# Optimization experiments

Measured on AMD Instinct MI355X. Metric: run time of the kernel, lower is better.

## Reference

```python
import jax, jax.numpy as jnp
import numpy as np

E = 8          # n_routed_experts
TOP_K = 2      # num_experts_per_tok
H = 1024       # hidden_size
I = 512        # moe_intermediate_size
SI = 512       # shared expert intermediate (I * n_shared_experts)
B, S = 4, 4096


def setup_inputs() -> dict:
    key = jax.random.key(0)
    ks = jax.random.split(key, 8)
    sc_h = 1.0 / np.sqrt(H)
    sc_i = 1.0 / np.sqrt(I)
    return {
        "hidden_states": jax.random.normal(ks[0], (B, S, H), jnp.float32),
        "gate_w": jax.random.normal(ks[1], (E, H), jnp.float32) * sc_h,  # router logits weight [E,H]
        "Wg": jax.random.normal(ks[2], (E, H, I), jnp.float32) * sc_h,   # per-expert gate_proj
        "Wu": jax.random.normal(ks[3], (E, H, I), jnp.float32) * sc_h,   # per-expert up_proj
        "Wd": jax.random.normal(ks[4], (E, I, H), jnp.float32) * sc_i,   # per-expert down_proj
        "sWg": jax.random.normal(ks[5], (H, SI), jnp.float32) * sc_h,    # shared expert gate_proj
        "sWu": jax.random.normal(ks[6], (H, SI), jnp.float32) * sc_h,
        "sWd": jax.random.normal(ks[7], (SI, H), jnp.float32) * sc_i,
    }


def reference(hidden_states, gate_w, Wg, Wu, Wd, sWg, sWu, sWd):
    b, s, h = hidden_states.shape
    x = hidden_states.reshape(-1, h)                      # [T,H]

    # ---- MoEGate: softmax scoring + greedy top-k + weight normalization ----
    logits = x.astype(jnp.float32) @ gate_w.T             # [T,E]
    scores = jax.nn.softmax(logits, axis=-1)
    topk_w, topk_idx = jax.lax.top_k(scores, TOP_K)       # [T,K]
    topk_w = topk_w / (topk_w.sum(-1, keepdims=True) + 1e-20)  # norm_topk_prob

    # combine weights as a dense [T,E] map (scatter of topk weights)
    cw = (jax.nn.one_hot(topk_idx, E, dtype=topk_w.dtype) * topk_w[..., None]).sum(1)  # [T,E]

    # ---- routed experts: down(gelu(gate(x)) * up(x)), combined by gate weight ----
    g = jnp.einsum("th,ehi->tei", x, Wg)
    u = jnp.einsum("th,ehi->tei", x, Wu)
    inter = jax.nn.gelu(g, approximate=False) * u         # [T,E,I]
    y = jnp.einsum("tei,te,eih->th", inter, cw.astype(x.dtype), Wd)

    # ---- shared expert on the identity path ----
    sh = (jax.nn.gelu(x @ sWg, approximate=False) * (x @ sWu)) @ sWd

    return (y + sh).reshape(b, s, h)
```

## Files before the change

### kernel.cpp

```cpp
#include <hip/hip_runtime.h>
#include <hip/hip_bf16.h>
#include <math.h>


#define T_TOTAL 16384
#define HDIM 1024
#define IDIM 512
#define NE 9
#define CNT_STRIDE 16
#define SH_BASE 32768

typedef __bf16 bf16x8 __attribute__((ext_vector_type(8)));
typedef float f32x4 __attribute__((ext_vector_type(4)));

typedef __attribute__((address_space(1))) void gvoid_t;
typedef __attribute__((address_space(3))) void lvoid_t;

__device__ __forceinline__ void load_lds16(const void* g, void* l) {
  __builtin_amdgcn_global_load_lds((const gvoid_t*)g, (lvoid_t*)l, 16, 0, 0);
}

__device__ __forceinline__ f32x4 mfma_bf16(bf16x8 a, bf16x8 b, f32x4 c) {
  return __builtin_amdgcn_mfma_f32_16x16x32_bf16(a, b, c, 0, 0, 0);
}

__global__ __launch_bounds__(256) void k_gate(const float* __restrict__ x,
                                              const float* __restrict__ gw,
                                              __bf16* __restrict__ xb,
                                              int* __restrict__ tok,
                                              float* __restrict__ wtl,
                                              int* __restrict__ cnt,
                                              int* __restrict__ inv) {
  __shared__ int s_eid[64][2];
  __shared__ float s_wt[64][2];
  __shared__ int s_rank[64][2];
  __shared__ int lcnt[8];
  __shared__ int lbase[8];
  const int wv = threadIdx.x >> 6, lane = threadIdx.x & 63;
  if (threadIdx.x < 8) lcnt[threadIdx.x] = 0;
  __syncthreads();

  for (int i = 0; i < 16; i++) {
    const int tl = wv * 16 + i;
    const int t = blockIdx.x * 64 + tl;
    const float* xr = x + (size_t)t * HDIM + lane * 16;
    float4 xv[4];
#pragma unroll
    for (int j = 0; j < 4; j++) xv[j] = ((const float4*)xr)[j];

    bf16x8 v0, v1;
#pragma unroll
    for (int j = 0; j < 8; j++) v0[j] = (__bf16)((const float*)xv)[j];
#pragma unroll
    for (int j = 0; j < 8; j++) v1[j] = (__bf16)((const float*)xv)[j + 8];
    bf16x8* xbo = (bf16x8*)(xb + (size_t)t * HDIM + lane * 16);
    xbo[0] = v0;
    xbo[1] = v1;

    float acc[8];
#pragma unroll
    for (int e = 0; e < 8; e++) {
      const float4* gp = (const float4*)(gw + e * HDIM + lane * 16);
      float s = 0.f;
#pragma unroll
      for (int j = 0; j < 4; j++) {
        float4 g = gp[j];
        s += xv[j].x * g.x + xv[j].y * g.y + xv[j].z * g.z + xv[j].w * g.w;
      }
      acc[e] = s;
    }
#pragma unroll
    for (int d = 32; d >= 1; d >>= 1) {
#pragma unroll
      for (int e = 0; e < 8; e++) acc[e] += __shfl_xor(acc[e], d, 64);
    }
    if (lane == 0) {
      float mx = acc[0];
#pragma unroll
      for (int e = 1; e < 8; e++) mx = fmaxf(mx, acc[e]);
      float p[8], Z = 0.f;
#pragma unroll
      for (int e = 0; e < 8; e++) {
        p[e] = expf(acc[e] - mx);
        Z += p[e];
      }
#pragma unroll
      for (int e = 0; e < 8; e++) p[e] /= Z;
      int i1 = 0;
#pragma unroll
      for (int e = 1; e < 8; e++)
        if (p[e] > p[i1]) i1 = e;
      int i2 = (i1 == 0) ? 1 : 0;
#pragma unroll
      for (int e = 0; e < 8; e++)
        if (e != i1 && p[e] > p[i2]) i2 = e;
      const float s12 = p[i1] + p[i2] + 1e-20f;
      s_eid[tl][0] = i1;
      s_eid[tl][1] = i2;
      s_wt[tl][0] = p[i1] / s12;
      s_wt[tl][1] = p[i2] / s12;
    }
  }
  __syncthreads();

  if (threadIdx.x < 64) {
    s_rank[threadIdx.x][0] = atomicAdd(&lcnt[s_eid[threadIdx.x][0]], 1);
    s_rank[threadIdx.x][1] = atomicAdd(&lcnt[s_eid[threadIdx.x][1]], 1);
  }
  __syncthreads();
  if (threadIdx.x < 8)
    lbase[threadIdx.x] =
        atomicAdd(&cnt[threadIdx.x * CNT_STRIDE], lcnt[threadIdx.x]);
  __syncthreads();
  if (threadIdx.x < 64) {
    const int t = blockIdx.x * 64 + threadIdx.x;
#pragma unroll
    for (int j = 0; j < 2; j++) {
      const int e = s_eid[threadIdx.x][j];
      const int slot = lbase[e] + s_rank[threadIdx.x][j];
      tok[e * T_TOTAL + slot] = t;
      wtl[e * T_TOTAL + slot] = s_wt[threadIdx.x][j];
      inv[t * 2 + j] = e * T_TOTAL + slot;
    }
  }
}

__global__ __launch_bounds__(256) void k_wprep(
    const float* __restrict__ Wg, const float* __restrict__ Wu,
    const float* __restrict__ Wd, const float* __restrict__ sWg,
    const float* __restrict__ sWu, const float* __restrict__ sWd,
    __bf16* __restrict__ Wfu, __bf16* __restrict__ WdT,
    const int* __restrict__ cnt, int* __restrict__ base) {
  if (blockIdx.z == 26 && blockIdx.x == 0 && blockIdx.y == 0 &&
      threadIdx.x == 0) {
    int s = 0;
#pragma unroll
    for (int e = 0; e < 8; e++) {
      base[e] = s;
      s += cnt[e * CNT_STRIDE];
    }
  }

  __shared__ float tile[64][65];
  const int z = blockIdx.z;
  const int t = threadIdx.x;

  if (z < 18) {
    if (blockIdx.x >= IDIM / 64) return;
    const int b = (z < 9) ? z : z - 9;
    const int u16off = (z < 9) ? 0 : 16;
    const float* w8 = (z < 9) ? Wg : Wu;
    const float* w1 = (z < 9) ? sWg : sWu;
    const float* src = (b < 8) ? (w8 + (size_t)b * HDIM * IDIM) : w1;
    const int c0 = blockIdx.x * 64, r0 = blockIdx.y * 64;

#pragma unroll
    for (int j = 0; j < 4; j++) {
      const int rr = (t >> 4) + j * 16;
      const int cc = (t & 15) * 4;
      const float4 v =
          *(const float4*)(src + (size_t)(r0 + rr) * IDIM + c0 + cc);
      tile[rr][cc] = v.x;
      tile[rr][cc + 1] = v.y;
      tile[rr][cc + 2] = v.z;
      tile[rr][cc + 3] = v.w;
    }
    __syncthreads();

#pragma unroll
    for (int j = 0; j < 2; j++) {
      const int cidx = (t >> 3) + j * 32;
      const int rseg = (t & 7) * 8;
      const int ic = c0 + cidx;
      const int f = 2 * (ic & ~15) + (ic & 15) + u16off;
      bf16x8 v;
#pragma unroll
      for (int k = 0; k < 8; k++) v[k] = (__bf16)tile[rseg + k][cidx];
      *(bf16x8*)(Wfu + (size_t)b * 1024 * HDIM + (size_t)f * HDIM + r0 + rseg) =
          v;
    }
  } else {
    if (blockIdx.y >= IDIM / 64) return;
    const int b = z - 18;
    const float* src = (b < 8) ? (Wd + (size_t)b * IDIM * HDIM) : sWd;
    const int c0 = blockIdx.x * 64, r0 = blockIdx.y * 64;

#pragma unroll
    for (int j = 0; j < 4; j++) {
      const int rr = (t >> 4) + j * 16;
      const int cc = (t & 15) * 4;
      const float4 v =
          *(const float4*)(src + (size_t)(r0 + rr) * HDIM + c0 + cc);
      tile[rr][cc] = v.x;
      tile[rr][cc + 1] = v.y;
      tile[rr][cc + 2] = v.z;
      tile[rr][cc + 3] = v.w;
    }
    __syncthreads();

#pragma unroll
    for (int j = 0; j < 2; j++) {
      const int cidx = (t >> 3) + j * 32;
      const int rseg = (t & 7) * 8;
      bf16x8 v;
#pragma unroll
      for (int k = 0; k < 8; k++) v[k] = (__bf16)tile[rseg + k][cidx];
      *(bf16x8*)(WdT + (size_t)b * HDIM * IDIM + (size_t)(c0 + cidx) * IDIM +
                 r0 + rseg) = v;
    }
  }
}

__global__ __launch_bounds__(256, 2) void k_gu(
    const __bf16* __restrict__ xb, const __bf16* __restrict__ Wfu,
    const int* __restrict__ tok, const float* __restrict__ wtl,
    const int* __restrict__ cnt, const int* __restrict__ base,
    __bf16* __restrict__ inter, int zbase) {
  const int e = blockIdx.z + zbase;
  const bool se = (e == 8);
  const int cnt_e = se ? T_TOTAL : cnt[e * CNT_STRIDE];
  const int m0 = blockIdx.x * 128;
  if (m0 >= cnt_e) return;
  const int rowb = se ? SH_BASE : base[e];

  __shared__ __bf16 sA[128][64];
  __shared__ __bf16 sB[128][64];
  const int tid = threadIdx.x, w = tid >> 6, lane = tid & 63;
  const int n0 = blockIdx.y * 128;
  const int quad = lane >> 4, l16 = lane & 15;
  const int wm = (w & 1) * 64, wn = (w >> 1) * 64;

  const int sr = tid >> 3;
  const int scs = ((tid & 7) ^ (sr & 7)) * 8;
  const __bf16* ap[4];
  const __bf16* bp[4];
#pragma unroll
  for (int sh = 0; sh < 4; sh++) {
    int s = m0 + sh * 32 + sr;
    if (s > cnt_e - 1) s = cnt_e - 1;
    const int t = se ? s : tok[e * T_TOTAL + s];
    ap[sh] = xb + (size_t)t * HDIM + scs;
    bp[sh] = Wfu + ((size_t)e * 1024 + n0 + sh * 32 + sr) * HDIM + scs;
  }
  char* const la = (char*)sA + w * 1024;
  char* const lb = (char*)sB + w * 1024;

  f32x4 acc[4][4];
#pragma unroll
  for (int im = 0; im < 4; im++)
#pragma unroll
    for (int in = 0; in < 4; in++) acc[im][in] = {0.f, 0.f, 0.f, 0.f};

  for (int k = 0; k < HDIM; k += 64) {
    __syncthreads();
#pragma unroll
    for (int sh = 0; sh < 4; sh++) {
      load_lds16(ap[sh], la + sh * 4096);
      load_lds16(bp[sh], lb + sh * 4096);
      ap[sh] += 64;
      bp[sh] += 64;
    }
    __syncthreads();
#pragma unroll
    for (int kh = 0; kh < 2; kh++) {
      bf16x8 af[4], bfr[4];
#pragma unroll
      for (int i = 0; i < 4; i++) {
        const int ra = wm + i * 16 + l16;
        af[i] = *(const bf16x8*)((const char*)sA + ra * 128 +
                                 ((kh * 4 + quad) ^ (ra & 7)) * 16);
        const int rb = wn + i * 16 + l16;
        bfr[i] = *(const bf16x8*)((const char*)sB + rb * 128 +
                                  ((kh * 4 + quad) ^ (rb & 7)) * 16);
      }
#pragma unroll
      for (int im = 0; im < 4; im++)
#pragma unroll
        for (int in = 0; in < 4; in++)
          acc[im][in] = mfma_bf16(af[im], bfr[in], acc[im][in]);
    }
  }

#pragma unroll
  for (int im = 0; im < 4; im++) {
#pragma unroll
    for (int r = 0; r < 4; r++) {
      const int slot = m0 + wm + im * 16 + quad * 4 + r;
      if (slot < cnt_e) {
        const float wt = se ? 1.0f : wtl[e * T_TOTAL + slot];
        __bf16* op =
            inter + ((size_t)(rowb + slot)) * IDIM + ((n0 + wn) >> 1) + l16;
#pragma unroll
        for (int p = 0; p < 2; p++) {
          const float g = acc[im][2 * p][r];
          const float u = acc[im][2 * p + 1][r];
          const float v =
              wt * u * 0.5f * g * (1.0f + erff(g * 0.70710678118654752f));
          op[p * 16] = (__bf16)v;
        }
      }
    }
  }
}

__global__ __launch_bounds__(256, 2) void k_down_rs(
    const __bf16* __restrict__ inter, const __bf16* __restrict__ WdT,
    const int* __restrict__ cnt, const int* __restrict__ base,
    f32x4* __restrict__ yb4) {
  const int e = blockIdx.z;
  const int cnt_e = cnt[e * CNT_STRIDE];
  const int m0 = blockIdx.x * 128;
  if (m0 >= cnt_e) return;
  const int rowb = base[e];

  __shared__ __bf16 sA[128][64];
  __shared__ __bf16 sB[128][64];
  const int tid = threadIdx.x, w = tid >> 6, lane = tid & 63;
  const int n0 = blockIdx.y * 128;
  const int quad = lane >> 4, l16 = lane & 15;
  const int wm = (w & 1) * 64, wn = (w >> 1) * 64;
  const int nseg = (n0 + wn) >> 6;

  const int sr = tid >> 3;
  const int scs = ((tid & 7) ^ (sr & 7)) * 8;
  const __bf16* ap[4];
  const __bf16* bp[4];
#pragma unroll
  for (int sh = 0; sh < 4; sh++) {
    int s = m0 + sh * 32 + sr;
    if (s > cnt_e - 1) s = cnt_e - 1;
    ap[sh] = inter + (size_t)(rowb + s) * IDIM + scs;
    bp[sh] = WdT + ((size_t)e * HDIM + n0 + sh * 32 + sr) * IDIM + scs;
  }
  char* const la = (char*)sA + w * 1024;
  char* const lb = (char*)sB + w * 1024;

  f32x4 acc[4][4];
#pragma unroll
  for (int im = 0; im < 4; im++)
#pragma unroll
    for (int in = 0; in < 4; in++) acc[im][in] = {0.f, 0.f, 0.f, 0.f};

  for (int k = 0; k < IDIM; k += 64) {
    __syncthreads();
#pragma unroll
    for (int sh = 0; sh < 4; sh++) {
      load_lds16(ap[sh], la + sh * 4096);
      load_lds16(bp[sh], lb + sh * 4096);
      ap[sh] += 64;
      bp[sh] += 64;
    }
    __syncthreads();
#pragma unroll
    for (int kh = 0; kh < 2; kh++) {
      bf16x8 af[4], bfr[4];
#pragma unroll
      for (int i = 0; i < 4; i++) {
        const int ra = wm + i * 16 + l16;
        af[i] = *(const bf16x8*)((const char*)sA + ra * 128 +
                                 ((kh * 4 + quad) ^ (ra & 7)) * 16);
        const int rb = wn + i * 16 + l16;
        bfr[i] = *(const bf16x8*)((const char*)sB + rb * 128 +
                                  ((kh * 4 + quad) ^ (rb & 7)) * 16);
      }
#pragma unroll
      for (int im = 0; im < 4; im++)
#pragma unroll
        for (int in = 0; in < 4; in++)
          acc[im][in] = mfma_bf16(af[im], bfr[in], acc[im][in]);
    }
  }

#pragma unroll
  for (int im = 0; im < 4; im++) {
#pragma unroll
    for (int r = 0; r < 4; r++) {
      const int slot = m0 + wm + im * 16 + quad * 4 + r;
      if (slot < cnt_e) {
        const size_t row = (size_t)(rowb + slot);
        f32x4 v = {acc[im][0][r], acc[im][1][r], acc[im][2][r], acc[im][3][r]};
        yb4[(row * 16 + nseg) * 16 + l16] = v;
      }
    }
  }
}

__global__ __launch_bounds__(256, 2) void k_down_sc(
    const __bf16* __restrict__ iA, const __bf16* __restrict__ wB,
    const f32x4* __restrict__ yb4, const int* __restrict__ inv,
    const int* __restrict__ base, float* __restrict__ out) {
  __shared__ __bf16 sA[128][64];
  __shared__ __bf16 sB[128][64];
  const int tid = threadIdx.x, w = tid >> 6, lane = tid & 63;
  const int m0 = blockIdx.x * 128, n0 = blockIdx.y * 128;
  const int quad = lane >> 4, l16 = lane & 15;
  const int wm = (w & 1) * 64, wn = (w >> 1) * 64;
  const int nseg = (n0 + wn) >> 6;

  const int sr = tid >> 3;
  const int scs = ((tid & 7) ^ (sr & 7)) * 8;
  const __bf16* ap[4];
  const __bf16* bp[4];
#pragma unroll
  for (int sh = 0; sh < 4; sh++) {
    ap[sh] = iA + (size_t)(m0 + sh * 32 + sr) * IDIM + scs;
    bp[sh] = wB + (size_t)(n0 + sh * 32 + sr) * IDIM + scs;
  }
  char* const la = (char*)sA + w * 1024;
  char* const lb = (char*)sB + w * 1024;

  f32x4 acc[4][4];
#pragma unroll
  for (int im = 0; im < 4; im++)
#pragma unroll
    for (int in = 0; in < 4; in++) acc[im][in] = {0.f, 0.f, 0.f, 0.f};

  for (int k = 0; k < IDIM; k += 64) {
    __syncthreads();
#pragma unroll
    for (int sh = 0; sh < 4; sh++) {
      load_lds16(ap[sh], la + sh * 4096);
      load_lds16(bp[sh], lb + sh * 4096);
      ap[sh] += 64;
      bp[sh] += 64;
    }
    __syncthreads();
#pragma unroll
    for (int kh = 0; kh < 2; kh++) {
      bf16x8 af[4], bfr[4];
#pragma unroll
      for (int i = 0; i < 4; i++) {
        const int ra = wm + i * 16 + l16;
        af[i] = *(const bf16x8*)((const char*)sA + ra * 128 +
                                 ((kh * 4 + quad) ^ (ra & 7)) * 16);
        const int rb = wn + i * 16 + l16;
        bfr[i] = *(const bf16x8*)((const char*)sB + rb * 128 +
                                  ((kh * 4 + quad) ^ (rb & 7)) * 16);
      }
#pragma unroll
      for (int im = 0; im < 4; im++)
#pragma unroll
        for (int in = 0; in < 4; in++)
          acc[im][in] = mfma_bf16(af[im], bfr[in], acc[im][in]);
    }
  }

#pragma unroll
  for (int im = 0; im < 4; im++) {
#pragma unroll
    for (int r = 0; r < 4; r++) {
      const int t = m0 + wm + im * 16 + quad * 4 + r;
      const int v1 = inv[2 * t], v2 = inv[2 * t + 1];
      const size_t r1 = base[v1 >> 14] + (v1 & (T_TOTAL - 1));
      const size_t r2 = base[v2 >> 14] + (v2 & (T_TOTAL - 1));
      const f32x4 y1 = yb4[(r1 * 16 + nseg) * 16 + l16];
      const f32x4 y2 = yb4[(r2 * 16 + nseg) * 16 + l16];
      float* op = out + (size_t)t * HDIM + n0 + wn + l16;
#pragma unroll
      for (int in = 0; in < 4; in++)
        op[in * 16] = acc[im][in][r] + y1[in] + y2[in];
    }
  }
}

__global__ __launch_bounds__(256, 2) void k_down_s(const __bf16* __restrict__ iA,
                                                   const __bf16* __restrict__ wB,
                                                   float* __restrict__ out) {
  __shared__ __bf16 sA[128][64];
  __shared__ __bf16 sB[128][64];
  const int tid = threadIdx.x, w = tid >> 6, lane = tid & 63;
  const int m0 = blockIdx.x * 128, n0 = blockIdx.y * 128;
  const int quad = lane >> 4, l16 = lane & 15;
  const int wm = (w & 1) * 64, wn = (w >> 1) * 64;

  const int sr = tid >> 3;
  const int scs = ((tid & 7) ^ (sr & 7)) * 8;
  const __bf16* ap[4];
  const __bf16* bp[4];
#pragma unroll
  for (int sh = 0; sh < 4; sh++) {
    ap[sh] = iA + (size_t)(m0 + sh * 32 + sr) * IDIM + scs;
    bp[sh] = wB + (size_t)(n0 + sh * 32 + sr) * IDIM + scs;
  }
  char* const la = (char*)sA + w * 1024;
  char* const lb = (char*)sB + w * 1024;

  f32x4 acc[4][4];
#pragma unroll
  for (int im = 0; im < 4; im++)
#pragma unroll
    for (int in = 0; in < 4; in++) acc[im][in] = {0.f, 0.f, 0.f, 0.f};

  for (int k = 0; k < IDIM; k += 64) {
    __syncthreads();
#pragma unroll
    for (int sh = 0; sh < 4; sh++) {
      load_lds16(ap[sh], la + sh * 4096);
      load_lds16(bp[sh], lb + sh * 4096);
      ap[sh] += 64;
      bp[sh] += 64;
    }
    __syncthreads();
#pragma unroll
    for (int kh = 0; kh < 2; kh++) {
      bf16x8 af[4], bfr[4];
#pragma unroll
      for (int i = 0; i < 4; i++) {
        const int ra = wm + i * 16 + l16;
        af[i] = *(const bf16x8*)((const char*)sA + ra * 128 +
                                 ((kh * 4 + quad) ^ (ra & 7)) * 16);
        const int rb = wn + i * 16 + l16;
        bfr[i] = *(const bf16x8*)((const char*)sB + rb * 128 +
                                  ((kh * 4 + quad) ^ (rb & 7)) * 16);
      }
#pragma unroll
      for (int im = 0; im < 4; im++)
#pragma unroll
        for (int in = 0; in < 4; in++)
          acc[im][in] = mfma_bf16(af[im], bfr[in], acc[im][in]);
    }
  }

#pragma unroll
  for (int im = 0; im < 4; im++) {
#pragma unroll
    for (int r = 0; r < 4; r++) {
      const int t = m0 + wm + im * 16 + quad * 4 + r;
#pragma unroll
      for (int in = 0; in < 4; in++)
        out[(size_t)t * HDIM + n0 + wn + in * 16 + l16] = acc[im][in][r];
    }
  }
}

__global__ __launch_bounds__(256, 2) void k_down_r(
    const __bf16* __restrict__ inter, const __bf16* __restrict__ WdT,
    const int* __restrict__ tok, const int* __restrict__ cnt,
    const int* __restrict__ base, float* __restrict__ out) {
  const int e = blockIdx.z;
  const int cnt_e = cnt[e * CNT_STRIDE];
  const int m0 = blockIdx.x * 128;
  if (m0 >= cnt_e) return;
  const int rowb = base[e];

  __shared__ __bf16 sA[128][64];
  __shared__ __bf16 sB[128][64];
  const int tid = threadIdx.x, w = tid >> 6, lane = tid & 63;
  const int n0 = blockIdx.y * 128;
  const int quad = lane >> 4, l16 = lane & 15;
  const int wm = (w & 1) * 64, wn = (w >> 1) * 64;

  const int sr = tid >> 3;
  const int scs = ((tid & 7) ^ (sr & 7)) * 8;
  const __bf16* ap[4];
  const __bf16* bp[4];
#pragma unroll
  for (int sh = 0; sh < 4; sh++) {
    int s = m0 + sh * 32 + sr;
    if (s > cnt_e - 1) s = cnt_e - 1;
    ap[sh] = inter + (size_t)(rowb + s) * IDIM + scs;
    bp[sh] = WdT + ((size_t)e * HDIM + n0 + sh * 32 + sr) * IDIM + scs;
  }
  char* const la = (char*)sA + w * 1024;
  char* const lb = (char*)sB + w * 1024;

  f32x4 acc[4][4];
#pragma unroll
  for (int im = 0; im < 4; im++)
#pragma unroll
    for (int in = 0; in < 4; in++) acc[im][in] = {0.f, 0.f, 0.f, 0.f};

  for (int k = 0; k < IDIM; k += 64) {
    __syncthreads();
#pragma unroll
    for (int sh = 0; sh < 4; sh++) {
      load_lds16(ap[sh], la + sh * 4096);
      load_lds16(bp[sh], lb + sh * 4096);
      ap[sh] += 64;
      bp[sh] += 64;
    }
    __syncthreads();
#pragma unroll
    for (int kh = 0; kh < 2; kh++) {
      bf16x8 af[4], bfr[4];
#pragma unroll
      for (int i = 0; i < 4; i++) {
        const int ra = wm + i * 16 + l16;
        af[i] = *(const bf16x8*)((const char*)sA + ra * 128 +
                                 ((kh * 4 + quad) ^ (ra & 7)) * 16);
        const int rb = wn + i * 16 + l16;
        bfr[i] = *(const bf16x8*)((const char*)sB + rb * 128 +
                                  ((kh * 4 + quad) ^ (rb & 7)) * 16);
      }
#pragma unroll
      for (int im = 0; im < 4; im++)
#pragma unroll
        for (int in = 0; in < 4; in++)
          acc[im][in] = mfma_bf16(af[im], bfr[in], acc[im][in]);
    }
  }

#pragma unroll
  for (int im = 0; im < 4; im++) {
#pragma unroll
    for (int r = 0; r < 4; r++) {
      const int slot = m0 + wm + im * 16 + quad * 4 + r;
      if (slot < cnt_e) {
        const int t = tok[e * T_TOTAL + slot];
#pragma unroll
        for (int in = 0; in < 4; in++)
          atomicAdd(&out[(size_t)t * HDIM + n0 + wn + in * 16 + l16],
                    acc[im][in][r]);
      }
    }
  }
}

extern "C" void kernel_launch(void* const* d_in, const int* in_sizes, int n_in,
                              void* d_out, int out_size, void* d_ws,
                              size_t ws_size, hipStream_t stream) {
  const float* x = (const float*)d_in[0];
  const float* gw = (const float*)d_in[1];
  const float* Wg = (const float*)d_in[2];
  const float* Wu = (const float*)d_in[3];
  const float* Wd = (const float*)d_in[4];
  const float* sWg = (const float*)d_in[5];
  const float* sWu = (const float*)d_in[6];
  const float* sWd = (const float*)d_in[7];
  float* out = (float*)d_out;

  char* ws = (char*)d_ws;
  size_t off = 0;
  auto alloc = [&](size_t n) {
    char* p = ws + off;
    off += (n + 255) & ~(size_t)255;
    return p;
  };
  __bf16* WdT = (__bf16*)alloc((size_t)NE * HDIM * IDIM * 2);
  int* tok = (int*)alloc((size_t)8 * T_TOTAL * 4);
  float* wtl = (float*)alloc((size_t)8 * T_TOTAL * 4);
  int* cnt = (int*)alloc(8 * CNT_STRIDE * 4);
  int* inv = (int*)alloc((size_t)T_TOTAL * 2 * 4);
  int* base = (int*)alloc(16 * 4);
  __bf16* inter = (__bf16*)alloc((size_t)(3 * T_TOTAL) * IDIM * 2);
  const size_t off_persist = off;
  __bf16* xb = (__bf16*)alloc((size_t)T_TOTAL * HDIM * 2);
  __bf16* Wfu = (__bf16*)alloc((size_t)NE * 1024 * HDIM * 2);

  const size_t yb_bytes = (size_t)2 * T_TOTAL * HDIM * 4;
  const bool store_path = (off_persist + yb_bytes) <= ws_size;
  f32x4* yb4 = (f32x4*)(ws + off_persist);

  hipMemsetAsync(cnt, 0, 8 * CNT_STRIDE * 4, stream);

  k_gate<<<dim3(T_TOTAL / 64), dim3(256), 0, stream>>>(x, gw, xb, tok, wtl,
                                                       cnt, inv);
  k_wprep<<<dim3(16, 16, 27), dim3(256), 0, stream>>>(Wg, Wu, Wd, sWg, sWu,
                                                      sWd, Wfu, WdT, cnt, base);

  k_gu<<<dim3(T_TOTAL / 128, 1024 / 128, 4), dim3(256), 0, stream>>>(
      xb, Wfu, tok, wtl, cnt, base, inter, 0);
  k_gu<<<dim3(T_TOTAL / 128, 1024 / 128, 4), dim3(256), 0, stream>>>(
      xb, Wfu, tok, wtl, cnt, base, inter, 4);
  k_gu<<<dim3(T_TOTAL / 128, 1024 / 128, 1), dim3(256), 0, stream>>>(
      xb, Wfu, tok, wtl, cnt, base, inter, 8);

  if (store_path) {
    k_down_rs<<<dim3(T_TOTAL / 128, HDIM / 128, 8), dim3(256), 0, stream>>>(
        inter, WdT, cnt, base, yb4);
    k_down_sc<<<dim3(T_TOTAL / 128, HDIM / 128), dim3(256), 0, stream>>>(
        inter + (size_t)SH_BASE * IDIM, WdT + (size_t)8 * HDIM * IDIM, yb4, inv,
        base, out);
  } else {
    k_down_s<<<dim3(T_TOTAL / 128, HDIM / 128), dim3(256), 0, stream>>>(
        inter + (size_t)SH_BASE * IDIM, WdT + (size_t)8 * HDIM * IDIM, out);
    k_down_r<<<dim3(T_TOTAL / 128, HDIM / 128, 8), dim3(256), 0, stream>>>(
        inter, WdT, tok, cnt, base, out);
  }
}
```

Baseline: 450.0 us.

## Scatter routed down-proj outputs by token slot and merge gate-up launches

Routed expert down-projection results are now written into a token-ordered buffer indexed by (token, k-slot), with the k-slot packed into the high bits of the tok array. The combine kernel no longer needs the inverse map or the base offsets, and it reads both expert contributions contiguously instead of gathering them. The three gate/up launches are merged into one grid over all nine experts. The trade-off is scattered writes in the routed kernel in exchange for coalesced reads in the combine step, plus one fewer index array and fewer launches.

```diff
diff --git a/kernel.cpp b/kernel.cpp
--- a/kernel.cpp
+++ b/kernel.cpp
@@ -29,8 +29,7 @@
                                               __bf16* __restrict__ xb,
                                               int* __restrict__ tok,
                                               float* __restrict__ wtl,
-                                              int* __restrict__ cnt,
-                                              int* __restrict__ inv) {
+                                              int* __restrict__ cnt) {
   __shared__ int s_eid[64][2];
   __shared__ float s_wt[64][2];
   __shared__ int s_rank[64][2];
@@ -118,9 +117,8 @@
     for (int j = 0; j < 2; j++) {
       const int e = s_eid[threadIdx.x][j];
       const int slot = lbase[e] + s_rank[threadIdx.x][j];
-      tok[e * T_TOTAL + slot] = t;
+      tok[e * T_TOTAL + slot] = t | (j << 14);
       wtl[e * T_TOTAL + slot] = s_wt[threadIdx.x][j];
-      inv[t * 2 + j] = e * T_TOTAL + slot;
     }
   }
 }
@@ -215,8 +213,8 @@
     const __bf16* __restrict__ xb, const __bf16* __restrict__ Wfu,
     const int* __restrict__ tok, const float* __restrict__ wtl,
     const int* __restrict__ cnt, const int* __restrict__ base,
-    __bf16* __restrict__ inter, int zbase) {
-  const int e = blockIdx.z + zbase;
+    __bf16* __restrict__ inter) {
+  const int e = blockIdx.z;
   const bool se = (e == 8);
   const int cnt_e = se ? T_TOTAL : cnt[e * CNT_STRIDE];
   const int m0 = blockIdx.x * 128;
@@ -238,7 +236,7 @@
   for (int sh = 0; sh < 4; sh++) {
     int s = m0 + sh * 32 + sr;
     if (s > cnt_e - 1) s = cnt_e - 1;
-    const int t = se ? s : tok[e * T_TOTAL + s];
+    const int t = se ? s : (tok[e * T_TOTAL + s] & (T_TOTAL - 1));
     ap[sh] = xb + (size_t)t * HDIM + scs;
     bp[sh] = Wfu + ((size_t)e * 1024 + n0 + sh * 32 + sr) * HDIM + scs;
   }
@@ -305,8 +303,8 @@
 
 __global__ __launch_bounds__(256, 2) void k_down_rs(
     const __bf16* __restrict__ inter, const __bf16* __restrict__ WdT,
-    const int* __restrict__ cnt, const int* __restrict__ base,
-    f32x4* __restrict__ yb4) {
+    const int* __restrict__ tok, const int* __restrict__ cnt,
+    const int* __restrict__ base, f32x4* __restrict__ ytok4) {
   const int e = blockIdx.z;
   const int cnt_e = cnt[e * CNT_STRIDE];
   const int m0 = blockIdx.x * 128;
@@ -377,9 +375,11 @@
     for (int r = 0; r < 4; r++) {
       const int slot = m0 + wm + im * 16 + quad * 4 + r;
       if (slot < cnt_e) {
-        const size_t row = (size_t)(rowb + slot);
+        const int tokv = tok[e * T_TOTAL + slot];
+        const size_t row =
+            2 * (size_t)(tokv & (T_TOTAL - 1)) + (tokv >> 14);
         f32x4 v = {acc[im][0][r], acc[im][1][r], acc[im][2][r], acc[im][3][r]};
-        yb4[(row * 16 + nseg) * 16 + l16] = v;
+        ytok4[((size_t)nseg * 32768 + row) * 16 + l16] = v;
       }
     }
   }
@@ -387,8 +387,7 @@
 
 __global__ __launch_bounds__(256, 2) void k_down_sc(
     const __bf16* __restrict__ iA, const __bf16* __restrict__ wB,
-    const f32x4* __restrict__ yb4, const int* __restrict__ inv,
-    const int* __restrict__ base, float* __restrict__ out) {
+    const f32x4* __restrict__ ytok4, float* __restrict__ out) {
   __shared__ __bf16 sA[128][64];
   __shared__ __bf16 sB[128][64];
   const int tid = threadIdx.x, w = tid >> 6, lane = tid & 63;
@@ -450,11 +449,8 @@
 #pragma unroll
     for (int r = 0; r < 4; r++) {
       const int t = m0 + wm + im * 16 + quad * 4 + r;
-      const int v1 = inv[2 * t], v2 = inv[2 * t + 1];
-      const size_t r1 = base[v1 >> 14] + (v1 & (T_TOTAL - 1));
-      const size_t r2 = base[v2 >> 14] + (v2 & (T_TOTAL - 1));
-      const f32x4 y1 = yb4[(r1 * 16 + nseg) * 16 + l16];
-      const f32x4 y2 = yb4[(r2 * 16 + nseg) * 16 + l16];
+      const f32x4 y1 = ytok4[((size_t)nseg * 32768 + 2 * t) * 16 + l16];
+      const f32x4 y2 = ytok4[((size_t)nseg * 32768 + 2 * t + 1) * 16 + l16];
       float* op = out + (size_t)t * HDIM + n0 + wn + l16;
 #pragma unroll
       for (int in = 0; in < 4; in++)
@@ -606,7 +602,7 @@
     for (int r = 0; r < 4; r++) {
       const int slot = m0 + wm + im * 16 + quad * 4 + r;
       if (slot < cnt_e) {
-        const int t = tok[e * T_TOTAL + slot];
+        const int t = tok[e * T_TOTAL + slot] & (T_TOTAL - 1);
 #pragma unroll
         for (int in = 0; in < 4; in++)
           atomicAdd(&out[(size_t)t * HDIM + n0 + wn + in * 16 + l16],
@@ -640,37 +636,32 @@
   int* tok = (int*)alloc((size_t)8 * T_TOTAL * 4);
   float* wtl = (float*)alloc((size_t)8 * T_TOTAL * 4);
   int* cnt = (int*)alloc(8 * CNT_STRIDE * 4);
-  int* inv = (int*)alloc((size_t)T_TOTAL * 2 * 4);
   int* base = (int*)alloc(16 * 4);
   __bf16* inter = (__bf16*)alloc((size_t)(3 * T_TOTAL) * IDIM * 2);
   const size_t off_persist = off;
   __bf16* xb = (__bf16*)alloc((size_t)T_TOTAL * HDIM * 2);
   __bf16* Wfu = (__bf16*)alloc((size_t)NE * 1024 * HDIM * 2);
 
-  const size_t yb_bytes = (size_t)2 * T_TOTAL * HDIM * 4;
-  const bool store_path = (off_persist + yb_bytes) <= ws_size;
-  f32x4* yb4 = (f32x4*)(ws + off_persist);
+  const size_t ytok_bytes = (size_t)2 * T_TOTAL * HDIM * 4;
+  const bool store_path = (off_persist + ytok_bytes) <= ws_size;
+  f32x4* ytok4 = (f32x4*)(ws + off_persist);
 
   hipMemsetAsync(cnt, 0, 8 * CNT_STRIDE * 4, stream);
 
   k_gate<<<dim3(T_TOTAL / 64), dim3(256), 0, stream>>>(x, gw, xb, tok, wtl,
-                                                       cnt, inv);
+                                                       cnt);
   k_wprep<<<dim3(16, 16, 27), dim3(256), 0, stream>>>(Wg, Wu, Wd, sWg, sWu,
                                                       sWd, Wfu, WdT, cnt, base);
 
-  k_gu<<<dim3(T_TOTAL / 128, 1024 / 128, 4), dim3(256), 0, stream>>>(
-      xb, Wfu, tok, wtl, cnt, base, inter, 0);
-  k_gu<<<dim3(T_TOTAL / 128, 1024 / 128, 4), dim3(256), 0, stream>>>(
-      xb, Wfu, tok, wtl, cnt, base, inter, 4);
-  k_gu<<<dim3(T_TOTAL / 128, 1024 / 128, 1), dim3(256), 0, stream>>>(
-      xb, Wfu, tok, wtl, cnt, base, inter, 8);
+  k_gu<<<dim3(T_TOTAL / 128, 1024 / 128, NE), dim3(256), 0, stream>>>(
+      xb, Wfu, tok, wtl, cnt, base, inter);
 
   if (store_path) {
     k_down_rs<<<dim3(T_TOTAL / 128, HDIM / 128, 8), dim3(256), 0, stream>>>(
-        inter, WdT, cnt, base, yb4);
+        inter, WdT, tok, cnt, base, ytok4);
     k_down_sc<<<dim3(T_TOTAL / 128, HDIM / 128), dim3(256), 0, stream>>>(
-        inter + (size_t)SH_BASE * IDIM, WdT + (size_t)8 * HDIM * IDIM, yb4, inv,
-        base, out);
+        inter + (size_t)SH_BASE * IDIM, WdT + (size_t)8 * HDIM * IDIM, ytok4,
+        out);
   } else {
     k_down_s<<<dim3(T_TOTAL / 128, HDIM / 128), dim3(256), 0, stream>>>(
         inter + (size_t)SH_BASE * IDIM, WdT + (size_t)8 * HDIM * IDIM, out);
```

Result: no change. 441.6 us (-1.9%).
